# Kernel tuning notes

Measured on AMD Instinct MI355X. Metric: run time of the kernel, lower is better.

## Reference

```python
import jax, jax.numpy as jnp
import numpy as np

N_OPS = 8  # eset_ops_3_to_3: identity, 3 single-axis sums, 3 pair sums, full sum (broadcast back)


def _conv(x, w, b):
    # x: (N,C,H,W), w: (O,C,kh,kw), VALID conv, stride 1
    y = jax.lax.conv_general_dilated(x, w, (1, 1), 'VALID',
                                     dimension_numbers=('NCHW', 'OIHW', 'NCHW'))
    return y + b[None, :, None, None]


def _maxpool2(x):
    return jax.lax.reduce_window(x, -jnp.inf, jax.lax.max,
                                 (1, 1, 2, 2), (1, 1, 2, 2), 'VALID')


def _eq3to3(x, W, b):
    # x: (B,i,j,k,d) channels-last; W: (N_OPS,d,o); b: (o,)
    # Fused form: contract each summed basis op with its weight BEFORE broadcasting.
    si = x.sum(1)          # (B,j,k,d)
    sj = x.sum(2)          # (B,i,k,d)
    sk = x.sum(3)          # (B,i,j,d)
    sij = x.sum((1, 2))    # (B,k,d)
    sik = x.sum((1, 3))    # (B,j,d)
    sjk = x.sum((2, 3))    # (B,i,d)
    s = x.sum((1, 2, 3))   # (B,d)
    y = jnp.einsum('bijkd,do->bijko', x, W[0])
    y = y + jnp.einsum('bjkd,do->bjko', si, W[1])[:, None]
    y = y + jnp.einsum('bikd,do->biko', sj, W[2])[:, :, None]
    y = y + jnp.einsum('bijd,do->bijo', sk, W[3])[:, :, :, None]
    y = y + jnp.einsum('bkd,do->bko', sij, W[4])[:, None, None]
    y = y + jnp.einsum('bjd,do->bjo', sik, W[5])[:, None, :, None]
    y = y + jnp.einsum('bid,do->bio', sjk, W[6])[:, :, None, None]
    y = y + jnp.einsum('bd,do->bo', s, W[7])[:, None, None, None]
    return y + b


def setup_inputs() -> dict:
    key = jax.random.key(0)
    ks = jax.random.split(key, 14)
    B, k, h, w = 16, 40, 28, 28
    hid, out_dim = 64, 32
    flat = 64 * 4 * 4  # after conv5-pool2-conv5-pool2 on 28x28
    p = lambda ki, shape, fan: jax.random.normal(ki, shape, jnp.float32) / np.sqrt(fan)
    return {
        'x': jax.random.normal(ks[0], (B, k, h, w), jnp.float32),
        'conv1_w': p(ks[1], (32, 1, 5, 5), 25),
        'conv1_b': jnp.zeros((32,), jnp.float32),
        'conv2_w': p(ks[2], (64, 32, 5, 5), 32 * 25),
        'conv2_b': jnp.zeros((64,), jnp.float32),
        'fc_w': p(ks[3], (flat, hid), flat),
        'fc_b': jnp.zeros((hid,), jnp.float32),
        'eq1_w': p(ks[4], (N_OPS, hid, hid), N_OPS * hid) * 0.1,
        'eq1_b': jnp.zeros((hid,), jnp.float32),
        'eq2_w': p(ks[5], (N_OPS, hid, out_dim), N_OPS * hid) * 0.1,
        'eq2_b': jnp.zeros((out_dim,), jnp.float32),
        'out_w': p(ks[6], (out_dim, 1), out_dim),
        'out_b': jnp.zeros((1,), jnp.float32),
    }


def reference(x, conv1_w, conv1_b, conv2_w, conv2_b, fc_w, fc_b,
              eq1_w, eq1_b, eq2_w, eq2_b, out_w, out_b):
    B, k, h, w = x.shape
    z = x.reshape(B * k, 1, h, w)
    z = _maxpool2(jax.nn.relu(_conv(z, conv1_w, conv1_b)))
    z = _maxpool2(jax.nn.relu(_conv(z, conv2_w, conv2_b)))
    z = z.reshape(B * k, -1) @ fc_w + fc_b
    e = jax.nn.relu(z).reshape(B, k, -1)          # (B,k,d)
    t = jnp.einsum('bid,bjd,bkd->bijkd', e, e, e)  # (B,k,k,k,d) cubic tensor
    y = jax.nn.relu(_eq3to3(t, eq1_w, eq1_b))
    y = _eq3to3(y, eq2_w, eq2_b)                   # (B,k,k,k,out_dim)
    y = jax.nn.relu(y).sum(axis=(1, 2, 3))         # (B,out_dim); dropout_prob=0 (eval)
    y = jax.nn.relu(y)
    return y @ out_w + out_b                       # (B,1)
```

## Files before the change

### kernel.cpp

```cpp
#include <hip/hip_runtime.h>
#include <hip/hip_bf16.h>


typedef unsigned short u16;
typedef __attribute__((ext_vector_type(8))) short bf8_t;
typedef __attribute__((ext_vector_type(4))) float f4_t;

#define LSTR 72

__device__ inline u16 f2bf(float f){
  union { float f; unsigned u; } v; v.f = f;
  unsigned r = v.u + 0x7fffu + ((v.u >> 16) & 1u);
  return (u16)(r >> 16);
}
__device__ inline float bflo(unsigned u){ union { unsigned x; float f; } v; v.x = u << 16; return v.f; }
__device__ inline float bfhi(unsigned u){ union { unsigned x; float f; } v; v.x = u & 0xffff0000u; return v.f; }
__device__ inline unsigned pack2(float a, float b){ return (unsigned)f2bf(a) | ((unsigned)f2bf(b) << 16); }
__device__ inline unsigned cvtpk(float lo, float hi){
  __hip_bfloat162 h2 = __float22bfloat162_rn(make_float2(lo, hi));
  union { __hip_bfloat162 h; unsigned u; } c; c.h = h2; return c.u;
}
__device__ inline void unpack8(bf8_t x, float* o){
  union { bf8_t v; unsigned u[4]; } q; q.v = x;
  #pragma unroll
  for (int p = 0; p < 4; ++p){ o[2*p] = bflo(q.u[p]); o[2*p+1] = bfhi(q.u[p]); }
}
__device__ inline f4_t shfl4x(f4_t v, int m){
  f4_t r;
  r[0] = __shfl_xor(v[0], m); r[1] = __shfl_xor(v[1], m);
  r[2] = __shfl_xor(v[2], m); r[3] = __shfl_xor(v[3], m);
  return r;
}

__global__ __launch_bounds__(256) void kconv1(const float* __restrict__ x, const float* __restrict__ w1,
                                              const float* __restrict__ b1, u16* __restrict__ z1t,
                                              const float* __restrict__ w2, const float* __restrict__ fcw,
                                              u16* __restrict__ wt2, u16* __restrict__ fcwT){
  __shared__ float simg[784];
  int img = blockIdx.x, tid = threadIdx.x;
  if (img >= 640){
    int t = (img - 640)*256 + tid, stride = 32*256;
    for (int i = t; i < 51200; i += stride){
      int tap = i >> 11, rc = i & 2047, co = rc >> 5, ci = rc & 31;
      wt2[i] = f2bf(w2[co*800 + ci*25 + tap]);
    }
    for (int i = t; i < 65536; i += stride){
      int o = i >> 10, k = i & 1023;
      fcwT[i] = f2bf(fcw[k*64 + o]);
    }
    return;
  }
  for (int i = tid; i < 784; i += 256) simg[i] = x[img*784 + i];
  const int c = tid & 31;
  float wc[25];
  #pragma unroll
  for (int t = 0; t < 25; ++t) wc[t] = w1[c*25 + t];
  const float bb = b1[c];
  __syncthreads();
  #pragma unroll 2
  for (int it = 0; it < 18; ++it){
    int p = (tid >> 5) + it*8;
    int py = p / 12, px = p % 12;
    float patch[36];
    const float* sp = &simg[2*py*28 + 2*px];
    #pragma unroll
    for (int yy = 0; yy < 6; ++yy)
      #pragma unroll
      for (int xx = 0; xx < 6; ++xx) patch[yy*6+xx] = sp[yy*28+xx];
    float mx = -1e30f;
    #pragma unroll
    for (int sy = 0; sy < 2; ++sy)
    #pragma unroll
    for (int sx = 0; sx < 2; ++sx){
      float s = bb;
      #pragma unroll
      for (int dy = 0; dy < 5; ++dy)
        #pragma unroll
        for (int dx = 0; dx < 5; ++dx)
          s += patch[(sy+dy)*6 + sx+dx] * wc[dy*5+dx];
      mx = fmaxf(mx, s);
    }
    z1t[(size_t)img*4608 + p*32 + c] = f2bf(fmaxf(mx, 0.f));
  }
}

__global__ __launch_bounds__(256) void kconv2m(const u16* __restrict__ z1t, const u16* __restrict__ wt2,
                                               const float* __restrict__ b2, u16* __restrict__ z2g){
  __shared__ __align__(16) u16 sz[4608];
  __shared__ __align__(16) u16 sz2[1024];
  int img = blockIdx.x, tid = threadIdx.x;
  for (int i = tid; i < 576; i += 256)
    ((uint4*)sz)[i] = ((const uint4*)(z1t + (size_t)img*4608))[i];
  __syncthreads();
  const int wave = tid >> 6, lane = tid & 63, l15 = lane & 15, quad = lane >> 4;
  const int y = wave*2 + (l15 >> 3), x = l15 & 7;
  f4_t acc[4];
  acc[0] = (f4_t){0.f,0.f,0.f,0.f}; acc[1] = acc[0]; acc[2] = acc[0]; acc[3] = acc[0];
  #pragma unroll
  for (int dy = 0; dy < 5; ++dy)
    #pragma unroll
    for (int dx = 0; dx < 5; ++dx){
      const int tap = dy*5 + dx;
      bf8_t af = *(const bf8_t*)&sz[((y+dy)*12 + (x+dx))*32 + quad*8];
      const u16* wp = wt2 + tap*2048 + l15*32 + quad*8;
      #pragma unroll
      for (int nt = 0; nt < 4; ++nt){
        bf8_t bf = *(const bf8_t*)(wp + nt*512);
        acc[nt] = __builtin_amdgcn_mfma_f32_16x16x32_bf16(af, bf, acc[nt], 0, 0, 0);
      }
    }
  #pragma unroll
  for (int nt = 0; nt < 4; ++nt){
    int co = nt*16 + l15;
    float v0 = fmaxf(acc[nt][0], acc[nt][1]);
    float v1 = fmaxf(acc[nt][2], acc[nt][3]);
    v0 = fmaxf(v0, __shfl_xor(v0, 32));
    v1 = fmaxf(v1, __shfl_xor(v1, 32));
    if (quad < 2){
      float bb = b2[co];
      sz2[co*16 + wave*4 + quad*2 + 0] = f2bf(fmaxf(v0 + bb, 0.f));
      sz2[co*16 + wave*4 + quad*2 + 1] = f2bf(fmaxf(v1 + bb, 0.f));
    }
  }
  __syncthreads();
  if (tid < 128) ((uint4*)(z2g + (size_t)img*1024))[tid] = ((const uint4*)sz2)[tid];
}

__global__ __launch_bounds__(256) void kfc(const u16* __restrict__ z2g, const u16* __restrict__ fcwT,
                                           const float* __restrict__ fcb,
                                           float* __restrict__ e_f, u16* __restrict__ e_b){
  __shared__ __align__(16) u16 sA[16*1032];
  int img0 = blockIdx.x*16, tid = threadIdx.x;
  for (int i = tid; i < 2048; i += 256){
    int row = i >> 7, c16 = i & 127;
    ((uint4*)(sA + row*1032))[c16] = ((const uint4*)(z2g + (size_t)(img0+row)*1024))[c16];
  }
  __syncthreads();
  const int wave = tid >> 6, lane = tid & 63, l15 = lane & 15, quad = lane >> 4;
  const int o = wave*16 + l15;
  f4_t acc = (f4_t){0.f,0.f,0.f,0.f};
  #pragma unroll 8
  for (int ks = 0; ks < 32; ++ks){
    bf8_t af = *(const bf8_t*)&sA[l15*1032 + ks*32 + quad*8];
    bf8_t bf = *(const bf8_t*)(fcwT + (size_t)o*1024 + ks*32 + quad*8);
    acc = __builtin_amdgcn_mfma_f32_16x16x32_bf16(af, bf, acc, 0, 0, 0);
  }
  const float bb = fcb[o];
  #pragma unroll
  for (int r = 0; r < 4; ++r){
    int img = img0 + quad*4 + r;
    float v = fmaxf(acc[r] + bb, 0.f);
    e_f[img*64 + o] = v;
    e_b[img*64 + o] = f2bf(v);
  }
}

__global__ __launch_bounds__(256) void kprep(const float* __restrict__ e_f, const float* __restrict__ e1w,
    const float* __restrict__ e1b, const float* __restrict__ e2w,
    float* __restrict__ Sg, u16* __restrict__ Vt, float* __restrict__ c0,
    float* __restrict__ P5, float* __restrict__ P6, u16* __restrict__ W2T0,
    u16* __restrict__ W3St){
  int b = blockIdx.x, ph = blockIdx.y, tid = threadIdx.x;
  __shared__ float se[2560];
  __shared__ float S[64], S2[64], S3[64];
  for (int i = tid; i < 2560; i += 256) se[i] = e_f[b*2560 + i];
  __syncthreads();
  if (tid < 64){
    float s = 0.f;
    for (int i = 0; i < 40; ++i) s += se[i*64 + tid];
    S[tid] = s; S2[tid] = s*s; S3[tid] = s*s*s;
    if (ph == 0) Sg[b*64 + tid] = s;
  }
  __syncthreads();
  {
    const int m = ph;
    for (int idx = tid; idx < 4096; idx += 256){
      int o = idx >> 6, d = idx & 63;
      float v;
      if (m == 0)      v = e1w[d*64 + o];
      else if (m == 1) v = S[d] * e1w[4096  + d*64 + o];
      else if (m == 2) v = S[d] * e1w[8192  + d*64 + o];
      else             v = S2[d] * e1w[16384 + d*64 + o];
      Vt[(size_t)b*16384 + m*4096 + idx] = f2bf(v);
    }
  }
  if (ph == 0){
    if (tid < 64){
      float a = e1b[tid];
      for (int d = 0; d < 64; ++d) a += S3[d] * e1w[7*4096 + d*64 + tid];
      c0[b*64 + tid] = a;
    }
  } else if (ph == 1){
    for (int idx = tid; idx < 4096; idx += 256){
      int o = idx >> 6, d = idx & 63;
      W3St[(size_t)b*4096 + idx] = f2bf(S[d] * e1w[3*4096 + d*64 + o]);
    }
  } else {
    int lo = (ph == 2) ? 0 : 1280, hi = lo + 1280;
    for (int idx = lo + tid; idx < hi; idx += 256){
      int j = idx >> 6, o = idx & 63;
      float a5 = 0.f, a6 = 0.f;
      for (int d = 0; d < 64; ++d){
        float es = se[j*64 + d] * S2[d];
        a5 += es * e1w[5*4096 + d*64 + o];
        a6 += es * e1w[6*4096 + d*64 + o];
      }
      P5[(b*40+j)*64 + o] = a5;
      P6[(b*40+j)*64 + o] = a6;
    }
    if (ph == 3 && b == 0){
      for (int idx = tid; idx < 2048; idx += 256){
        int o = idx >> 6, d = idx & 63;
        W2T0[o*64 + d] = f2bf(e2w[d*32 + o]);
      }
    }
  }
}

__global__ __launch_bounds__(256) void kpq(const u16* __restrict__ e_b, const u16* __restrict__ W3St,
    const float* __restrict__ P5, const float* __restrict__ P6, const float* __restrict__ c0,
    float* __restrict__ Q3c){
  __shared__ __align__(16) u16 sP[48*LSTR];
  __shared__ __align__(16) u16 sW[64*LSTR];
  int blk = blockIdx.x, b = blk/40, i = blk%40, tid = threadIdx.x;
  const int wave = tid >> 6, lane = tid & 63, l15 = lane & 15, quad = lane >> 4;
  for (int idx = tid; idx < 2048; idx += 256){
    int o = idx >> 5, c = idx & 31;
    ((unsigned*)(sW + o*LSTR))[c] = ((const unsigned*)(W3St + (size_t)b*4096))[idx];
  }
  const unsigned* eb32 = (const unsigned*)(e_b + (size_t)b*2560);
  const unsigned* el = eb32 + i*32;
  #pragma unroll
  for (int it = 0; it < 6; ++it){
    int idx = tid + it*256;
    int k = idx >> 5, d2 = idx & 31;
    unsigned pv = 0;
    if (k < 40){
      unsigned ul = el[d2], uk = eb32[k*32 + d2];
      pv = pack2(bflo(ul)*bflo(uk), bfhi(ul)*bfhi(uk));
    }
    ((unsigned*)(sP + k*LSTR))[d2] = pv;
  }
  __syncthreads();
  bf8_t wf[2];
  #pragma unroll
  for (int ks = 0; ks < 2; ++ks)
    wf[ks] = *(const bf8_t*)&sW[(wave*16 + l15)*LSTR + ks*32 + quad*8];
  f4_t acc[3];
  #pragma unroll
  for (int n = 0; n < 3; ++n){
    f4_t a = (f4_t){0.f,0.f,0.f,0.f};
    #pragma unroll
    for (int ks = 0; ks < 2; ++ks){
      bf8_t pkf = *(const bf8_t*)&sP[(n*16 + l15)*LSTR + ks*32 + quad*8];
      a = __builtin_amdgcn_mfma_f32_16x16x32_bf16(wf[ks], pkf, a, 0, 0, 0);
    }
    acc[n] = a;
  }
  const int obase = wave*16 + quad*4;
  f4_t p6v = *(const f4_t*)&P6[(b*40+i)*64 + obase];
  f4_t c0v = *(const f4_t*)&c0[b*64 + obase];
  #pragma unroll
  for (int n = 0; n < 3; ++n){
    int j = n*16 + l15;
    if (j < 40){
      f4_t p5v = *(const f4_t*)&P5[(b*40+j)*64 + obase];
      f4_t outv = acc[n] + p5v + p6v + c0v;
      *(f4_t*)&Q3c[((size_t)((b*40+i)*40 + j))*64 + obase] = outv;
    }
  }
}

__global__ __launch_bounds__(256, 4) void kh01(
    const u16* __restrict__ e_b, const float* __restrict__ e_f,
    const u16* __restrict__ Vt, const float* __restrict__ Q3c,
    float* __restrict__ si2, float* __restrict__ sj2, float* __restrict__ sk2)
{
  __shared__ __align__(16) char smem[25344];
  u16*   sU  = (u16*)smem;
  u16*   sB1 = (u16*)(smem + 6912);
  u16*   sB0 = (u16*)(smem + 16128);
  float* sUf = (float*)smem;
  const int tid = threadIdx.x;
  const int b = blockIdx.x / 40, fix = blockIdx.x % 40;
  const int mode = blockIdx.y;
  const int wave = tid >> 6, lane = tid & 63, l15 = lane & 15, quad = lane >> 4;
  const f4_t z4 = (f4_t){0.f,0.f,0.f,0.f};

  for (int idx = tid; idx < 1536; idx += 256){
    int r = idx >> 5, c = idx & 31;
    unsigned v = (r < 40) ? ((const unsigned*)e_b)[(b*40 + r)*32 + c] : 0u;
    ((unsigned*)(sU + r*LSTR))[c] = v;
  }
  float efr[10];
  #pragma unroll
  for (int t = 0; t < 10; ++t) efr[t] = e_f[b*2560 + tid + t*256];
  const unsigned* eg = (const unsigned*)(e_b + (size_t)(b*40 + fix)*64);
  const unsigned* Vb = (const unsigned*)(Vt + (size_t)b*16384);
  for (int idx = tid; idx < 2048; idx += 256){
    int o = idx >> 5, d2 = idx & 31;
    unsigned eu = eg[d2];
    unsigned v0 = Vb[o*32 + d2];
    unsigned vA = Vb[(2-mode)*2048 + o*32 + d2];
    unsigned vB = Vb[(1+mode)*2048 + o*32 + d2];
    unsigned v3 = Vb[3*2048 + o*32 + d2];
    float e0 = bflo(eu), e1 = bfhi(eu);
    ((unsigned*)(sB1 + o*LSTR))[d2] = pack2(e0*bflo(v0)+bflo(vA), e1*bfhi(v0)+bfhi(vA));
    ((unsigned*)(sB0 + o*LSTR))[d2] = pack2(e0*bflo(vB)+bflo(v3), e1*bfhi(vB)+bfhi(v3));
  }
  __syncthreads();

  f4_t b1v[4];
  bf8_t ua[3][2];
  f4_t Y0[3];
  {
    bf8_t b0f[2], b1f[2];
    float tmp[8];
    #pragma unroll
    for (int ks = 0; ks < 2; ++ks){
      b1f[ks] = *(const bf8_t*)&sB1[(wave*16 + l15)*LSTR + ks*32 + quad*8];
      b0f[ks] = *(const bf8_t*)&sB0[(wave*16 + l15)*LSTR + ks*32 + quad*8];
      unpack8(b1f[ks], tmp);
      b1v[2*ks]   = (f4_t){tmp[0],tmp[1],tmp[2],tmp[3]};
      b1v[2*ks+1] = (f4_t){tmp[4],tmp[5],tmp[6],tmp[7]};
    }
    #pragma unroll
    for (int n = 0; n < 3; ++n){
      f4_t a = z4;
      #pragma unroll
      for (int ks = 0; ks < 2; ++ks){
        ua[n][ks] = *(const bf8_t*)&sU[(n*16 + l15)*LSTR + ks*32 + quad*8];
        a = __builtin_amdgcn_mfma_f32_16x16x32_bf16(b0f[ks], ua[n][ks], a, 0, 0, 0);
      }
      Y0[n] = a;
    }
  }
  __syncthreads();
  #pragma unroll
  for (int t = 0; t < 10; ++t) sUf[tid + t*256] = efr[t];
  __syncthreads();

  const int obase = wave*16 + quad*4;
  const float km = (l15 < 8) ? 1.f : 0.f;
  const f4_t km4 = (f4_t){km, km, km, km};
  f4_t sacc[3];
  sacc[0] = z4; sacc[1] = z4; sacc[2] = z4;

  const int qstride = mode ? 64 : 2560;
  const float* qp = Q3c + (size_t)b*102400 + (mode ? (size_t)fix*2560 : (size_t)fix*64) + obase;
  float* skp = sk2 + ((size_t)(b*40)*40 + fix)*64 + obase;
  const float* ep = sUf + quad*8;

  f4_t cadd_n = *(const f4_t*)qp; qp += qstride;
  #pragma unroll 2
  for (int l = 0; l < 40; ++l){
    f4_t cadd = cadd_n;
    if (l < 39){ cadd_n = *(const f4_t*)qp; qp += qstride; }
    f4_t p00 = b1v[0] * *(const f4_t*)(ep);
    f4_t p01 = b1v[1] * *(const f4_t*)(ep + 4);
    f4_t p10 = b1v[2] * *(const f4_t*)(ep + 32);
    f4_t p11 = b1v[3] * *(const f4_t*)(ep + 36);
    ep += 64;
    union { bf8_t v; unsigned u[4]; } m0, m1;
    m0.u[0] = cvtpk(p00[0], p00[1]); m0.u[1] = cvtpk(p00[2], p00[3]);
    m0.u[2] = cvtpk(p01[0], p01[1]); m0.u[3] = cvtpk(p01[2], p01[3]);
    m1.u[0] = cvtpk(p10[0], p10[1]); m1.u[1] = cvtpk(p10[2], p10[3]);
    m1.u[2] = cvtpk(p11[0], p11[1]); m1.u[3] = cvtpk(p11[2], p11[3]);
    f4_t khs = z4;
    #pragma unroll
    for (int n = 0; n < 3; ++n){
      f4_t a = Y0[n];
      a = __builtin_amdgcn_mfma_f32_16x16x32_bf16(m0.v, ua[n][0], a, 0, 0, 0);
      a = __builtin_amdgcn_mfma_f32_16x16x32_bf16(m1.v, ua[n][1], a, 0, 0, 0);
      f4_t h = __builtin_elementwise_max(a + cadd, z4);
      sacc[n] += h;
      if (mode == 0) khs += (n == 2) ? h * km4 : h;
    }
    if (mode == 0){
      khs += shfl4x(khs, 1);
      khs += shfl4x(khs, 2);
      khs += shfl4x(khs, 4);
      khs += shfl4x(khs, 8);
      if (l15 == 0) *(f4_t*)skp = khs;
      skp += 2560;
    }
  }
  float* dst = mode ? sj2 : si2;
  #pragma unroll
  for (int n = 0; n < 3; ++n){
    int k = n*16 + l15;
    if (k < 40)
      *(f4_t*)&dst[((size_t)((b*40 + fix)*40 + k))*64 + obase] = sacc[n];
  }
}

__global__ __launch_bounds__(256) void k5ar(const float* __restrict__ si2, const float* __restrict__ sj2,
    float* __restrict__ ssij, float* __restrict__ ssik, float* __restrict__ ssjk){
  int b = blockIdx.x, which = blockIdx.y, half = blockIdx.z, tid = threadIdx.x;
  int base = half*1280;
  for (int idx = base + tid; idx < base + 1280; idx += 256){
    int r = idx >> 6, d = idx & 63;
    float a = 0.f;
    if (which == 0){
      for (int j = 0; j < 40; ++j) a += si2[((size_t)(b*40+j)*40 + r)*64 + d];
      ssij[b*2560 + idx] = a;
    } else if (which == 1){
      const float* p = &si2[(size_t)(b*40+r)*2560 + d];
      for (int k = 0; k < 40; ++k) a += p[k*64];
      ssik[b*2560 + idx] = a;
    } else {
      const float* q = &sj2[(size_t)(b*40+r)*2560 + d];
      for (int k = 0; k < 40; ++k) a += q[k*64];
      ssjk[b*2560 + idx] = a;
    }
  }
}

__global__ __launch_bounds__(256) void k5am(const float* __restrict__ ssij, const float* __restrict__ ssik,
    const float* __restrict__ ssjk, const float* __restrict__ e2w, const float* __restrict__ e2b,
    float* __restrict__ A4, float* __restrict__ A5, float* __restrict__ A6, float* __restrict__ A7){
  int b = blockIdx.x, half = blockIdx.y, tid = threadIdx.x;
  __shared__ float s1[2560], s2[2560], ss2[64];
  if (half == 0){
    for (int i = tid; i < 2560; i += 256) s1[i] = ssij[b*2560 + i];
    __syncthreads();
    if (tid < 64){
      float a = 0.f;
      for (int k = 0; k < 40; ++k) a += s1[k*64 + tid];
      ss2[tid] = a;
    }
    __syncthreads();
    for (int idx = tid; idx < 1280; idx += 256){
      int k = idx >> 5, o = idx & 31;
      float a4 = 0.f;
      for (int d = 0; d < 64; ++d) a4 += s1[k*64+d] * e2w[4*2048 + d*32 + o];
      A4[(b*40+k)*32 + o] = a4;
    }
    if (tid < 32){
      float a = e2b[tid];
      for (int d = 0; d < 64; ++d) a += ss2[d] * e2w[7*2048 + d*32 + tid];
      A7[b*32 + tid] = a;
    }
  } else {
    for (int i = tid; i < 2560; i += 256){ s1[i] = ssik[b*2560 + i]; s2[i] = ssjk[b*2560 + i]; }
    __syncthreads();
    for (int idx = tid; idx < 1280; idx += 256){
      int k = idx >> 5, o = idx & 31;
      float a5 = 0.f, a6 = 0.f;
      for (int d = 0; d < 64; ++d){
        a5 += s1[k*64+d] * e2w[5*2048 + d*32 + o];
        a6 += s2[k*64+d] * e2w[6*2048 + d*32 + o];
      }
      A5[(b*40+k)*32 + o] = a5;
      A6[(b*40+k)*32 + o] = a6;
    }
  }
}

__global__ __launch_bounds__(256) void k5b(const float* __restrict__ si2, const float* __restrict__ sj2,
    const float* __restrict__ sk2, const float* __restrict__ e2w,
    const float* __restrict__ A4, const float* __restrict__ A5, const float* __restrict__ A6,
    const float* __restrict__ A7,
    float* __restrict__ A1p, float* __restrict__ A2t, float* __restrict__ Cc){
  int which = blockIdx.y;
  int blk = blockIdx.x, b = blk/40, f = blk%40, tid = threadIdx.x;
  __shared__ __align__(16) f4_t ssrc[640];
  __shared__ __align__(16) f4_t swt[32*17];
  const float* S = (which == 0) ? si2 : (which == 1) ? sj2 : sk2;
  int wop = which + 1;
  const f4_t* Sg4 = (const f4_t*)&S[(size_t)(b*40+f)*2560];
  for (int idx = tid; idx < 640; idx += 256) ssrc[idx] = Sg4[idx];
  for (int idx = tid; idx < 512; idx += 256){
    int o = idx >> 4, d4 = idx & 15;
    f4_t w;
    #pragma unroll
    for (int r = 0; r < 4; ++r) w[r] = e2w[wop*2048 + (4*d4+r)*32 + o];
    swt[o*17 + d4] = w;
  }
  __syncthreads();
  const int o = tid & 31, rb = tid >> 5;
  float acc[5] = {0.f, 0.f, 0.f, 0.f, 0.f};
  #pragma unroll 4
  for (int d4 = 0; d4 < 16; ++d4){
    f4_t w = swt[o*17 + d4];
    #pragma unroll
    for (int it = 0; it < 5; ++it){
      f4_t s = ssrc[(rb + 8*it)*16 + d4];
      acc[it] += s[0]*w[0] + s[1]*w[1] + s[2]*w[2] + s[3]*w[3];
    }
  }
  #pragma unroll
  for (int it = 0; it < 5; ++it){
    int r = rb + 8*it;
    size_t oi = ((size_t)(b*40+f)*40 + r)*32 + o;
    float a = acc[it];
    if (which == 0)      A1p[oi] = a + A4[(b*40+r)*32 + o];
    else if (which == 1) A2t[oi] = a;
    else                 Cc[oi]  = a + A5[(b*40+r)*32 + o] + A6[(b*40+f)*32 + o] + A7[b*32 + o];
  }
}

__global__ __launch_bounds__(256, 3) void kh2(
    const u16* __restrict__ e_b, const float* __restrict__ e_f,
    const u16* __restrict__ Vt, const float* __restrict__ Q3c, const u16* __restrict__ W2T0,
    const float* __restrict__ A1p, const float* __restrict__ A2t, const float* __restrict__ Cc,
    float* __restrict__ out_part)
{
  __shared__ __align__(16) char smem[30080];
  u16*   sB1 = (u16*)smem;
  u16*   sB0 = (u16*)(smem + 9216);
  u16*   sU  = (u16*)(smem + 18432);
  u16*   sW2 = (u16*)(smem + 18432 + 6912);
  float* sUf = (float*)(smem + 18432);
  float* soacc = (float*)(smem + 29952);
  const int tid = threadIdx.x;
  const int b = blockIdx.x / 40, fix = blockIdx.x % 40;
  const int wave = tid >> 6, lane = tid & 63, l15 = lane & 15, quad = lane >> 4;
  const f4_t z4 = (f4_t){0.f,0.f,0.f,0.f};

  for (int idx = tid; idx < 1536; idx += 256){
    int r = idx >> 5, c = idx & 31;
    unsigned v = (r < 40) ? ((const unsigned*)e_b)[(b*40 + r)*32 + c] : 0u;
    ((unsigned*)(sU + r*LSTR))[c] = v;
  }
  float efr[10];
  #pragma unroll
  for (int t = 0; t < 10; ++t) efr[t] = e_f[b*2560 + tid + t*256];
  const unsigned* eg = (const unsigned*)(e_b + (size_t)(b*40 + fix)*64);
  const unsigned* Vb = (const unsigned*)(Vt + (size_t)b*16384);
  for (int idx = tid; idx < 2048; idx += 256){
    int o = idx >> 5, d2 = idx & 31;
    unsigned eu = eg[d2];
    unsigned v0 = Vb[o*32 + d2];
    unsigned vA = Vb[2*2048 + o*32 + d2];
    unsigned vB = Vb[1*2048 + o*32 + d2];
    unsigned v3 = Vb[3*2048 + o*32 + d2];
    float e0 = bflo(eu), e1 = bfhi(eu);
    ((unsigned*)(sB1 + o*LSTR))[d2] = pack2(e0*bflo(v0)+bflo(vA), e1*bfhi(v0)+bfhi(vA));
    ((unsigned*)(sB0 + o*LSTR))[d2] = pack2(e0*bflo(vB)+bflo(v3), e1*bfhi(vB)+bfhi(v3));
  }
  for (int idx = tid; idx < 1024; idx += 256){
    int o = idx >> 5, c = idx & 31;
    ((unsigned*)(sW2 + o*LSTR))[c] = ((const unsigned*)W2T0)[idx];
  }
  if (tid < 32) soacc[tid] = 0.f;
  __syncthreads();

  f4_t b1v[4];
  bf8_t ua[3][2], wfA[2][2];
  f4_t Y0[3];
  {
    bf8_t b0f[2], b1f[2];
    float tmp[8];
    #pragma unroll
    for (int ks = 0; ks < 2; ++ks){
      b1f[ks] = *(const bf8_t*)&sB1[(wave*16 + l15)*LSTR + ks*32 + quad*8];
      b0f[ks] = *(const bf8_t*)&sB0[(wave*16 + l15)*LSTR + ks*32 + quad*8];
      unpack8(b1f[ks], tmp);
      b1v[2*ks]   = (f4_t){tmp[0],tmp[1],tmp[2],tmp[3]};
      b1v[2*ks+1] = (f4_t){tmp[4],tmp[5],tmp[6],tmp[7]};
      #pragma unroll
      for (int m = 0; m < 2; ++m)
        wfA[m][ks] = *(const bf8_t*)&sW2[(m*16 + l15)*LSTR + ks*32 + quad*8];
    }
    #pragma unroll
    for (int n = 0; n < 3; ++n){
      f4_t a = z4;
      #pragma unroll
      for (int ks = 0; ks < 2; ++ks){
        ua[n][ks] = *(const bf8_t*)&sU[(n*16 + l15)*LSTR + ks*32 + quad*8];
        a = __builtin_amdgcn_mfma_f32_16x16x32_bf16(b0f[ks], ua[n][ks], a, 0, 0, 0);
      }
      Y0[n] = a;
    }
  }
  __syncthreads();
  #pragma unroll
  for (int t = 0; t < 10; ++t) sUf[tid + t*256] = efr[t];
  __syncthreads();

  const int obase = wave*16 + quad*4;
  const int o2b   = quad*4;
  const int kme   = wave*16 + l15;
  const int kmc   = kme < 40 ? kme : 39;
  const bool kval = (kme < 40) & (wave < 3);
  f4_t pa1[2], psum[2];
  psum[0] = z4; psum[1] = z4;
  if (wave < 3){
    #pragma unroll
    for (int m = 0; m < 2; ++m)
      pa1[m] = *(const f4_t*)&A1p[((size_t)((b*40 + fix)*40 + kmc))*32 + m*16 + o2b];
  }

  const float* qp  = Q3c + (size_t)b*102400 + (size_t)fix*64 + obase;
  const float* a2p = A2t + ((size_t)b*1600 + kmc)*32 + o2b;
  const float* ccp = Cc  + ((size_t)b*1600 + fix)*32 + o2b;
  const float* ep  = sUf + quad*8;

  f4_t cadd_n = *(const f4_t*)qp; qp += 2560;
  #pragma unroll 2
  for (int l = 0; l < 40; ++l){
    f4_t cadd = cadd_n;
    if (l < 39){ cadd_n = *(const f4_t*)qp; qp += 2560; }
    f4_t a2v[2], ccv[2];
    if (wave < 3){
      a2v[0] = *(const f4_t*)(a2p);      a2v[1] = *(const f4_t*)(a2p + 16);
      ccv[0] = *(const f4_t*)(ccp);      ccv[1] = *(const f4_t*)(ccp + 16);
    }
    a2p += 1280; ccp += 1280;
    f4_t p00 = b1v[0] * *(const f4_t*)(ep);
    f4_t p01 = b1v[1] * *(const f4_t*)(ep + 4);
    f4_t p10 = b1v[2] * *(const f4_t*)(ep + 32);
    f4_t p11 = b1v[3] * *(const f4_t*)(ep + 36);
    ep += 64;
    union { bf8_t v; unsigned u[4]; } m0, m1;
    m0.u[0] = cvtpk(p00[0], p00[1]); m0.u[1] = cvtpk(p00[2], p00[3]);
    m0.u[2] = cvtpk(p01[0], p01[1]); m0.u[3] = cvtpk(p01[2], p01[3]);
    m1.u[0] = cvtpk(p10[0], p10[1]); m1.u[1] = cvtpk(p10[2], p10[3]);
    m1.u[2] = cvtpk(p11[0], p11[1]); m1.u[3] = cvtpk(p11[2], p11[3]);
    u16* Hb = (u16*)(smem + (l & 1)*9216);
    #pragma unroll
    for (int n = 0; n < 3; ++n){
      f4_t a = Y0[n];
      a = __builtin_amdgcn_mfma_f32_16x16x32_bf16(m0.v, ua[n][0], a, 0, 0, 0);
      a = __builtin_amdgcn_mfma_f32_16x16x32_bf16(m1.v, ua[n][1], a, 0, 0, 0);
      f4_t h = __builtin_elementwise_max(a + cadd, z4);
      uint2 pw;
      pw.x = cvtpk(h[0], h[1]);
      pw.y = cvtpk(h[2], h[3]);
      *(uint2*)&Hb[(n*16 + l15)*LSTR + obase] = pw;
    }
    __syncthreads();
    if (wave < 3){
      bf8_t hB[2];
      #pragma unroll
      for (int ks = 0; ks < 2; ++ks)
        hB[ks] = *(const bf8_t*)&Hb[(wave*16 + l15)*LSTR + ks*32 + quad*8];
      #pragma unroll
      for (int m = 0; m < 2; ++m){
        f4_t y = z4;
        y = __builtin_amdgcn_mfma_f32_16x16x32_bf16(wfA[m][0], hB[0], y, 0, 0, 0);
        y = __builtin_amdgcn_mfma_f32_16x16x32_bf16(wfA[m][1], hB[1], y, 0, 0, 0);
        if (kval){
          f4_t v = y + pa1[m] + a2v[m] + ccv[m];
          psum[m] += __builtin_elementwise_max(v, z4);
        }
      }
    }
  }

  if (wave < 3){
    #pragma unroll
    for (int m = 0; m < 2; ++m){
      f4_t v = psum[m];
      v += shfl4x(v, 1); v += shfl4x(v, 2); v += shfl4x(v, 4); v += shfl4x(v, 8);
      if (l15 == 0){
        #pragma unroll
        for (int r = 0; r < 4; ++r) atomicAdd(&soacc[m*16 + o2b + r], v[r]);
      }
    }
  }
  __syncthreads();
  if (tid < 32) out_part[(b*40 + fix)*32 + tid] = soacc[tid];
}

__global__ __launch_bounds__(512) void k7(const float* __restrict__ out_part, const float* __restrict__ ow,
                                          const float* __restrict__ ob, float* __restrict__ out){
  int tid = threadIdx.x;
  int b = tid >> 5, o = tid & 31;
  float s = 0.f;
  for (int j = 0; j < 40; ++j) s += out_part[(b*40 + j)*32 + o];
  s = s > 0.f ? s : 0.f;
  float v = s * ow[o];
  v += __shfl_xor(v, 1); v += __shfl_xor(v, 2); v += __shfl_xor(v, 4);
  v += __shfl_xor(v, 8); v += __shfl_xor(v, 16);
  if (o == 0) out[b] = v + ob[0];
}

extern "C" void kernel_launch(void* const* d_in, const int* in_sizes, int n_in,
                              void* d_out, int out_size, void* d_ws, size_t ws_size,
                              hipStream_t stream){
  const float* x    = (const float*)d_in[0];
  const float* c1w  = (const float*)d_in[1];
  const float* c1b  = (const float*)d_in[2];
  const float* c2w  = (const float*)d_in[3];
  const float* c2b  = (const float*)d_in[4];
  const float* fcw  = (const float*)d_in[5];
  const float* fcb  = (const float*)d_in[6];
  const float* e1w  = (const float*)d_in[7];
  const float* e1b  = (const float*)d_in[8];
  const float* e2w  = (const float*)d_in[9];
  const float* e2b  = (const float*)d_in[10];
  const float* ow   = (const float*)d_in[11];
  const float* ob   = (const float*)d_in[12];

  char* ws = (char*)d_ws;
  size_t off = 0;
  auto alloc = [&](size_t bytes) -> void* {
    void* p = ws + off;
    off += (bytes + 255) & ~(size_t)255;
    return p;
  };
  u16*   z1t  = (u16*)  alloc((size_t)640*4608*2);
  u16*   wt2  = (u16*)  alloc(51200*2);
  u16*   fcwT = (u16*)  alloc(65536*2);
  u16*   z2g  = (u16*)  alloc((size_t)640*1024*2);
  float* e_f  = (float*)alloc(40960*4);
  u16*   e_b  = (u16*)  alloc(40960*2);
  float* Sg   = (float*)alloc(1024*4);
  u16*   Vt   = (u16*)  alloc((size_t)16*16384*2);
  float* c0   = (float*)alloc(1024*4);
  float* P5   = (float*)alloc(40960*4);
  float* P6   = (float*)alloc(40960*4);
  u16*   W2T0 = (u16*)  alloc(2048*2);
  u16*   W3St = (u16*)  alloc((size_t)16*4096*2);
  float* Q3c  = (float*)alloc((size_t)1638400*4);
  float* si2  = (float*)alloc((size_t)1638400*4);
  float* sj2  = (float*)alloc((size_t)1638400*4);
  float* sk2  = (float*)alloc((size_t)1638400*4);
  float* ssij = (float*)alloc(40960*4);
  float* ssik = (float*)alloc(40960*4);
  float* ssjk = (float*)alloc(40960*4);
  float* A4   = (float*)alloc(20480*4);
  float* A5   = (float*)alloc(20480*4);
  float* A6   = (float*)alloc(20480*4);
  float* A7   = (float*)alloc(512*4);
  float* A1p  = (float*)alloc((size_t)819200*4);
  float* A2t  = (float*)alloc((size_t)819200*4);
  float* Cc   = (float*)alloc((size_t)819200*4);
  float* op   = (float*)alloc(20480*4);
  (void)in_sizes; (void)n_in; (void)out_size; (void)ws_size;

  kconv1 <<<672, 256, 0, stream>>>(x, c1w, c1b, z1t, c2w, fcw, wt2, fcwT);
  kconv2m<<<640, 256, 0, stream>>>(z1t, wt2, c2b, z2g);
  kfc    <<<40,  256, 0, stream>>>(z2g, fcwT, fcb, e_f, e_b);
  kprep  <<<dim3(16,4), 256, 0, stream>>>(e_f, e1w, e1b, e2w, Sg, Vt, c0, P5, P6, W2T0, W3St);
  kpq    <<<640, 256, 0, stream>>>(e_b, W3St, P5, P6, c0, Q3c);
  kh01   <<<dim3(640,2), 256, 0, stream>>>(e_b, e_f, Vt, Q3c, si2, sj2, sk2);
  k5ar   <<<dim3(16,3,2), 256, 0, stream>>>(si2, sj2, ssij, ssik, ssjk);
  k5am   <<<dim3(16,2), 256, 0, stream>>>(ssij, ssik, ssjk, e2w, e2b, A4, A5, A6, A7);
  k5b    <<<dim3(640,3), 256, 0, stream>>>(si2, sj2, sk2, e2w, A4, A5, A6, A7, A1p, A2t, Cc);
  kh2    <<<640, 256, 0, stream>>>(e_b, e_f, Vt, Q3c, W2T0, A1p, A2t, Cc, op);
  k7     <<<1, 512, 0, stream>>>(op, ow, ob, (float*)d_out);
}
```

Before: 279.1 us.

## Split the l-loop across two wave groups in kh01 and kh2

Both heavy kernels now launch 512 threads per block, and the two groups of four waves each handle half of the 40-step l loop. Partial sums are combined through shared memory in kh01, while kh2 gets separate double-buffered H tiles per group and its shared memory grows to hold them. The aim is more waves in flight to hide latency and a shorter serial loop per wave. The cost is an extra reduction step plus block-wide barriers that now synchronise eight waves, and more LDS per block.

```diff
diff --git a/kernel.cpp b/kernel.cpp
--- a/kernel.cpp
+++ b/kernel.cpp
@@ -271,7 +271,7 @@
   }
 }
 
-__global__ __launch_bounds__(256, 4) void kh01(
+__global__ __launch_bounds__(512, 8) void kh01(
     const u16* __restrict__ e_b, const float* __restrict__ e_f,
     const u16* __restrict__ Vt, const float* __restrict__ Q3c,
     float* __restrict__ si2, float* __restrict__ sj2, float* __restrict__ sk2)
@@ -281,23 +281,26 @@
   u16*   sB1 = (u16*)(smem + 6912);
   u16*   sB0 = (u16*)(smem + 16128);
   float* sUf = (float*)smem;
+  float* sAcc = (float*)(smem + 10240);
   const int tid = threadIdx.x;
   const int b = blockIdx.x / 40, fix = blockIdx.x % 40;
   const int mode = blockIdx.y;
   const int wave = tid >> 6, lane = tid & 63, l15 = lane & 15, quad = lane >> 4;
+  const int g = wave >> 2, w4 = wave & 3;
+  const int lbeg = g*20;
   const f4_t z4 = (f4_t){0.f,0.f,0.f,0.f};
 
-  for (int idx = tid; idx < 1536; idx += 256){
+  for (int idx = tid; idx < 1536; idx += 512){
     int r = idx >> 5, c = idx & 31;
     unsigned v = (r < 40) ? ((const unsigned*)e_b)[(b*40 + r)*32 + c] : 0u;
     ((unsigned*)(sU + r*LSTR))[c] = v;
   }
-  float efr[10];
-  #pragma unroll
-  for (int t = 0; t < 10; ++t) efr[t] = e_f[b*2560 + tid + t*256];
+  float efr[5];
+  #pragma unroll
+  for (int t = 0; t < 5; ++t) efr[t] = e_f[b*2560 + tid + t*512];
   const unsigned* eg = (const unsigned*)(e_b + (size_t)(b*40 + fix)*64);
   const unsigned* Vb = (const unsigned*)(Vt + (size_t)b*16384);
-  for (int idx = tid; idx < 2048; idx += 256){
+  for (int idx = tid; idx < 2048; idx += 512){
     int o = idx >> 5, d2 = idx & 31;
     unsigned eu = eg[d2];
     unsigned v0 = Vb[o*32 + d2];
@@ -318,8 +321,8 @@
     float tmp[8];
     #pragma unroll
     for (int ks = 0; ks < 2; ++ks){
-      b1f[ks] = *(const bf8_t*)&sB1[(wave*16 + l15)*LSTR + ks*32 + quad*8];
-      b0f[ks] = *(const bf8_t*)&sB0[(wave*16 + l15)*LSTR + ks*32 + quad*8];
+      b1f[ks] = *(const bf8_t*)&sB1[(w4*16 + l15)*LSTR + ks*32 + quad*8];
+      b0f[ks] = *(const bf8_t*)&sB0[(w4*16 + l15)*LSTR + ks*32 + quad*8];
       unpack8(b1f[ks], tmp);
       b1v[2*ks]   = (f4_t){tmp[0],tmp[1],tmp[2],tmp[3]};
       b1v[2*ks+1] = (f4_t){tmp[4],tmp[5],tmp[6],tmp[7]};
@@ -337,25 +340,26 @@
   }
   __syncthreads();
   #pragma unroll
-  for (int t = 0; t < 10; ++t) sUf[tid + t*256] = efr[t];
-  __syncthreads();
-
-  const int obase = wave*16 + quad*4;
+  for (int t = 0; t < 5; ++t) sUf[tid + t*512] = efr[t];
+  __syncthreads();
+
+  const int obase = w4*16 + quad*4;
   const float km = (l15 < 8) ? 1.f : 0.f;
   const f4_t km4 = (f4_t){km, km, km, km};
   f4_t sacc[3];
   sacc[0] = z4; sacc[1] = z4; sacc[2] = z4;
 
   const int qstride = mode ? 64 : 2560;
-  const float* qp = Q3c + (size_t)b*102400 + (mode ? (size_t)fix*2560 : (size_t)fix*64) + obase;
-  float* skp = sk2 + ((size_t)(b*40)*40 + fix)*64 + obase;
-  const float* ep = sUf + quad*8;
+  const float* qp = Q3c + (size_t)b*102400 + (mode ? (size_t)fix*2560 : (size_t)fix*64)
+                    + (size_t)lbeg*qstride + obase;
+  float* skp = sk2 + ((size_t)((b*40 + lbeg)*40) + fix)*64 + obase;
+  const float* ep = sUf + lbeg*64 + quad*8;
 
   f4_t cadd_n = *(const f4_t*)qp; qp += qstride;
   #pragma unroll 2
-  for (int l = 0; l < 40; ++l){
+  for (int l = 0; l < 20; ++l){
     f4_t cadd = cadd_n;
-    if (l < 39){ cadd_n = *(const f4_t*)qp; qp += qstride; }
+    if (l < 19){ cadd_n = *(const f4_t*)qp; qp += qstride; }
     f4_t p00 = b1v[0] * *(const f4_t*)(ep);
     f4_t p01 = b1v[1] * *(const f4_t*)(ep + 4);
     f4_t p10 = b1v[2] * *(const f4_t*)(ep + 32);
@@ -385,12 +389,23 @@
       skp += 2560;
     }
   }
-  float* dst = mode ? sj2 : si2;
-  #pragma unroll
-  for (int n = 0; n < 3; ++n){
-    int k = n*16 + l15;
-    if (k < 40)
-      *(f4_t*)&dst[((size_t)((b*40 + fix)*40 + k))*64 + obase] = sacc[n];
+  __syncthreads();
+  if (g == 1){
+    #pragma unroll
+    for (int n = 0; n < 3; ++n)
+      *(f4_t*)&sAcc[(n*16 + l15)*68 + obase] = sacc[n];
+  }
+  __syncthreads();
+  if (g == 0){
+    float* dst = mode ? sj2 : si2;
+    #pragma unroll
+    for (int n = 0; n < 3; ++n){
+      int k = n*16 + l15;
+      if (k < 40){
+        f4_t ov = sacc[n] + *(const f4_t*)&sAcc[(n*16 + l15)*68 + obase];
+        *(f4_t*)&dst[((size_t)((b*40 + fix)*40 + k))*64 + obase] = ov;
+      }
+    }
   }
 }
 
@@ -500,35 +515,37 @@
   }
 }
 
-__global__ __launch_bounds__(256, 3) void kh2(
+__global__ __launch_bounds__(512, 6) void kh2(
     const u16* __restrict__ e_b, const float* __restrict__ e_f,
     const u16* __restrict__ Vt, const float* __restrict__ Q3c, const u16* __restrict__ W2T0,
     const float* __restrict__ A1p, const float* __restrict__ A2t, const float* __restrict__ Cc,
     float* __restrict__ out_part)
 {
-  __shared__ __align__(16) char smem[30080];
+  __shared__ __align__(16) char smem[48512];
   u16*   sB1 = (u16*)smem;
   u16*   sB0 = (u16*)(smem + 9216);
-  u16*   sU  = (u16*)(smem + 18432);
-  u16*   sW2 = (u16*)(smem + 18432 + 6912);
-  float* sUf = (float*)(smem + 18432);
-  float* soacc = (float*)(smem + 29952);
+  u16*   sU  = (u16*)(smem + 36864);
+  u16*   sW2 = (u16*)(smem + 36864 + 6912);
+  float* sUf = (float*)(smem + 36864);
+  float* soacc = (float*)(smem + 48384);
   const int tid = threadIdx.x;
   const int b = blockIdx.x / 40, fix = blockIdx.x % 40;
   const int wave = tid >> 6, lane = tid & 63, l15 = lane & 15, quad = lane >> 4;
+  const int g = wave >> 2, w4 = wave & 3;
+  const int lbeg = g*20;
   const f4_t z4 = (f4_t){0.f,0.f,0.f,0.f};
 
-  for (int idx = tid; idx < 1536; idx += 256){
+  for (int idx = tid; idx < 1536; idx += 512){
     int r = idx >> 5, c = idx & 31;
     unsigned v = (r < 40) ? ((const unsigned*)e_b)[(b*40 + r)*32 + c] : 0u;
     ((unsigned*)(sU + r*LSTR))[c] = v;
   }
-  float efr[10];
-  #pragma unroll
-  for (int t = 0; t < 10; ++t) efr[t] = e_f[b*2560 + tid + t*256];
+  float efr[5];
+  #pragma unroll
+  for (int t = 0; t < 5; ++t) efr[t] = e_f[b*2560 + tid + t*512];
   const unsigned* eg = (const unsigned*)(e_b + (size_t)(b*40 + fix)*64);
   const unsigned* Vb = (const unsigned*)(Vt + (size_t)b*16384);
-  for (int idx = tid; idx < 2048; idx += 256){
+  for (int idx = tid; idx < 2048; idx += 512){
     int o = idx >> 5, d2 = idx & 31;
     unsigned eu = eg[d2];
     unsigned v0 = Vb[o*32 + d2];
@@ -539,7 +556,7 @@
     ((unsigned*)(sB1 + o*LSTR))[d2] = pack2(e0*bflo(v0)+bflo(vA), e1*bfhi(v0)+bfhi(vA));
     ((unsigned*)(sB0 + o*LSTR))[d2] = pack2(e0*bflo(vB)+bflo(v3), e1*bfhi(vB)+bfhi(v3));
   }
-  for (int idx = tid; idx < 1024; idx += 256){
+  for (int idx = tid; idx < 1024; idx += 512){
     int o = idx >> 5, c = idx & 31;
     ((unsigned*)(sW2 + o*LSTR))[c] = ((const unsigned*)W2T0)[idx];
   }
@@ -554,8 +571,8 @@
     float tmp[8];
     #pragma unroll
     for (int ks = 0; ks < 2; ++ks){
-      b1f[ks] = *(const bf8_t*)&sB1[(wave*16 + l15)*LSTR + ks*32 + quad*8];
-      b0f[ks] = *(const bf8_t*)&sB0[(wave*16 + l15)*LSTR + ks*32 + quad*8];
+      b1f[ks] = *(const bf8_t*)&sB1[(w4*16 + l15)*LSTR + ks*32 + quad*8];
+      b0f[ks] = *(const bf8_t*)&sB0[(w4*16 + l15)*LSTR + ks*32 + quad*8];
       unpack8(b1f[ks], tmp);
       b1v[2*ks]   = (f4_t){tmp[0],tmp[1],tmp[2],tmp[3]};
       b1v[2*ks+1] = (f4_t){tmp[4],tmp[5],tmp[6],tmp[7]};
@@ -576,34 +593,34 @@
   }
   __syncthreads();
   #pragma unroll
-  for (int t = 0; t < 10; ++t) sUf[tid + t*256] = efr[t];
-  __syncthreads();
-
-  const int obase = wave*16 + quad*4;
+  for (int t = 0; t < 5; ++t) sUf[tid + t*512] = efr[t];
+  __syncthreads();
+
+  const int obase = w4*16 + quad*4;
   const int o2b   = quad*4;
-  const int kme   = wave*16 + l15;
+  const int kme   = w4*16 + l15;
   const int kmc   = kme < 40 ? kme : 39;
-  const bool kval = (kme < 40) & (wave < 3);
+  const bool kval = (kme < 40) & (w4 < 3);
   f4_t pa1[2], psum[2];
   psum[0] = z4; psum[1] = z4;
-  if (wave < 3){
+  if (w4 < 3){
     #pragma unroll
     for (int m = 0; m < 2; ++m)
       pa1[m] = *(const f4_t*)&A1p[((size_t)((b*40 + fix)*40 + kmc))*32 + m*16 + o2b];
   }
 
-  const float* qp  = Q3c + (size_t)b*102400 + (size_t)fix*64 + obase;
-  const float* a2p = A2t + ((size_t)b*1600 + kmc)*32 + o2b;
-  const float* ccp = Cc  + ((size_t)b*1600 + fix)*32 + o2b;
-  const float* ep  = sUf + quad*8;
+  const float* qp  = Q3c + (size_t)b*102400 + (size_t)fix*64 + (size_t)lbeg*2560 + obase;
+  const float* a2p = A2t + ((size_t)b*1600 + (size_t)lbeg*40 + kmc)*32 + o2b;
+  const float* ccp = Cc  + ((size_t)b*1600 + (size_t)lbeg*40 + fix)*32 + o2b;
+  const float* ep  = sUf + lbeg*64 + quad*8;
 
   f4_t cadd_n = *(const f4_t*)qp; qp += 2560;
   #pragma unroll 2
-  for (int l = 0; l < 40; ++l){
+  for (int l = 0; l < 20; ++l){
     f4_t cadd = cadd_n;
-    if (l < 39){ cadd_n = *(const f4_t*)qp; qp += 2560; }
+    if (l < 19){ cadd_n = *(const f4_t*)qp; qp += 2560; }
     f4_t a2v[2], ccv[2];
-    if (wave < 3){
+    if (w4 < 3){
       a2v[0] = *(const f4_t*)(a2p);      a2v[1] = *(const f4_t*)(a2p + 16);
       ccv[0] = *(const f4_t*)(ccp);      ccv[1] = *(const f4_t*)(ccp + 16);
     }
@@ -618,7 +635,7 @@
     m0.u[2] = cvtpk(p01[0], p01[1]); m0.u[3] = cvtpk(p01[2], p01[3]);
     m1.u[0] = cvtpk(p10[0], p10[1]); m1.u[1] = cvtpk(p10[2], p10[3]);
     m1.u[2] = cvtpk(p11[0], p11[1]); m1.u[3] = cvtpk(p11[2], p11[3]);
-    u16* Hb = (u16*)(smem + (l & 1)*9216);
+    u16* Hb = (u16*)(smem + (g*2 + (l & 1))*9216);
     #pragma unroll
     for (int n = 0; n < 3; ++n){
       f4_t a = Y0[n];
@@ -631,11 +648,11 @@
       *(uint2*)&Hb[(n*16 + l15)*LSTR + obase] = pw;
     }
     __syncthreads();
-    if (wave < 3){
+    if (w4 < 3){
       bf8_t hB[2];
       #pragma unroll
       for (int ks = 0; ks < 2; ++ks)
-        hB[ks] = *(const bf8_t*)&Hb[(wave*16 + l15)*LSTR + ks*32 + quad*8];
+        hB[ks] = *(const bf8_t*)&Hb[(w4*16 + l15)*LSTR + ks*32 + quad*8];
       #pragma unroll
       for (int m = 0; m < 2; ++m){
         f4_t y = z4;
@@ -649,7 +666,7 @@
     }
   }
 
-  if (wave < 3){
+  if (w4 < 3){
     #pragma unroll
     for (int m = 0; m < 2; ++m){
       f4_t v = psum[m];
@@ -736,10 +753,10 @@
   kfc    <<<40,  256, 0, stream>>>(z2g, fcwT, fcb, e_f, e_b);
   kprep  <<<dim3(16,4), 256, 0, stream>>>(e_f, e1w, e1b, e2w, Sg, Vt, c0, P5, P6, W2T0, W3St);
   kpq    <<<640, 256, 0, stream>>>(e_b, W3St, P5, P6, c0, Q3c);
-  kh01   <<<dim3(640,2), 256, 0, stream>>>(e_b, e_f, Vt, Q3c, si2, sj2, sk2);
+  kh01   <<<dim3(640,2), 512, 0, stream>>>(e_b, e_f, Vt, Q3c, si2, sj2, sk2);
   k5ar   <<<dim3(16,3,2), 256, 0, stream>>>(si2, sj2, ssij, ssik, ssjk);
   k5am   <<<dim3(16,2), 256, 0, stream>>>(ssij, ssik, ssjk, e2w, e2b, A4, A5, A6, A7);
   k5b    <<<dim3(640,3), 256, 0, stream>>>(si2, sj2, sk2, e2w, A4, A5, A6, A7, A1p, A2t, Cc);
-  kh2    <<<640, 256, 0, stream>>>(e_b, e_f, Vt, Q3c, W2T0, A1p, A2t, Cc, op);
+  kh2    <<<640, 512, 0, stream>>>(e_b, e_f, Vt, Q3c, W2T0, A1p, A2t, Cc, op);
   k7     <<<1, 512, 0, stream>>>(op, ow, ob, (float*)d_out);
 }
```

Result: slower. 885.5 us (+217.3%).
